# Performance work log

Hardware: AMD Instinct MI355X
Metric: run time of the kernel (lower is better)

## Reference

```python
import jax, jax.numpy as jnp
import numpy as np
from jax import lax

DT = 0.1
B, T, SD, CD, H = 1024, 200, 64, 32, 512


def setup_inputs() -> dict:
    key = jax.random.key(0)
    k0, k1, k2, k3 = jax.random.split(key, 4)
    scale1 = 1.0 / np.sqrt(SD + CD)
    scale2 = 1.0 / np.sqrt(H)
    return {
        "x0": jax.random.normal(k0, (B, SD), dtype=jnp.float32),
        "controls": jax.random.normal(k1, (B, T, CD), dtype=jnp.float32),
        "W1": jax.random.normal(k2, (SD + CD, H), dtype=jnp.float32) * scale1,
        "b1": jnp.zeros((H,), dtype=jnp.float32),
        "W2": jax.random.normal(k3, (H, SD), dtype=jnp.float32) * scale2,
        "b2": jnp.zeros((SD,), dtype=jnp.float32),
    }


def reference(x0, controls, W1, b1, W2, b2):
    # dynamics: x_{t+1} = x + dt * MLP(concat(x, u)); rollout with true data dependency
    def step(x, u):
        h = jnp.tanh(jnp.concatenate([x, u], axis=-1) @ W1 + b1)  # [B, H]
        x_next = x + DT * (h @ W2 + b2)                           # [B, SD]
        return x_next, x_next

    controls_t = jnp.swapaxes(controls, 0, 1)  # [T, B, CD]
    _, xs = lax.scan(step, x0, controls_t)     # xs: [T, B, SD]
    states = jnp.concatenate([x0[:, None, :], jnp.swapaxes(xs, 0, 1)], axis=1)  # [B, T+1, SD]
    return states
```

## Files before the change

kernel.cpp:

```cpp
#include <hip/hip_runtime.h>
#include <cstddef>


constexpr int B_  = 1024;
constexpr int T_  = 200;
constexpr int SD_ = 64;
constexpr int CD_ = 32;
constexpr int H_  = 512;
constexpr int KD_ = SD_ + CD_;
constexpr float DT_ = 0.1f;
constexpr int ROWS_ = 4;
constexpr int THREADS_ = 1024;
constexpr int KSLICES_ = 8;
constexpr int KLEN_ = KD_ / KSLICES_;

typedef float f2 __attribute__((ext_vector_type(2)));

__global__ __launch_bounds__(THREADS_)
void rollout_r15_kernel(
    const float* __restrict__ x0,
    const float* __restrict__ ctrl,
    const float* __restrict__ W1,
    const float* __restrict__ b1,
    const float* __restrict__ W2,
    const float* __restrict__ b2,
    float* __restrict__ out)
{
    __shared__ __align__(16) float xcT[KD_][ROWS_];
    __shared__ __align__(16) float part1[KSLICES_][ROWS_][H_];
    __shared__ __align__(16) float pbuf[ROWS_][H_];
    __shared__ __align__(16) float part2[ROWS_][32][SD_];

    const int tid = threadIdx.x;
    const int r0  = blockIdx.x * ROWS_;

    const int jpg   = tid & 127;
    const int ks    = tid >> 7;
    const int j0    = jpg * 2;
    const int kbase = ks * KLEN_;
    f2 w1a[KLEN_], w1b[KLEN_];
    #pragma unroll
    for (int i = 0; i < KLEN_; ++i) {
        w1a[i] = *(const f2*)&W1[(size_t)(kbase + i) * H_ + j0];
        w1b[i] = *(const f2*)&W1[(size_t)(kbase + i) * H_ + j0 + 256];
    }

    const int wv    = tid >> 6;
    const int lane  = tid & 63;
    const int l5    = lane >> 5;
    const int sfp   = lane & 31;
    const int sf0   = sfp * 2;
    const int hbase = wv * 32 + l5 * 16;
    f2 w2p[16];
    #pragma unroll
    for (int i = 0; i < 16; ++i)
        w2p[i] = *(const f2*)&W2[(size_t)(hbase + i) * SD_ + sf0];

    const int rF  = tid >> 8;
    const int jjF = (tid & 255) * 2;
    const f2 bj2 = {b1[jjF], b1[jjF + 1]};

    const int rf = (tid >> 6) & 3;
    const int sf = tid & 63;
    const float bs = b2[sf];

    const int  lt = tid - 512;
    const bool loader = (lt >= 0) && (lt < ROWS_ * CD_);
    const int  lr = (lt >> 5) & 3;
    const int  lc = lt & 31;
    const size_t ctrl_base = (size_t)(r0 + lr) * T_ * CD_ + lc;

    if (tid < ROWS_ * SD_) {
        const float v = x0[(size_t)(r0 + rf) * SD_ + sf];
        xcT[sf][rf] = v;
        out[(size_t)(r0 + rf) * (T_ + 1) * SD_ + sf] = v;
    }
    if (loader) xcT[SD_ + lc][lr] = ctrl[ctrl_base];
    __syncthreads();

    for (int t = 0; t < T_; ++t) {
        float cpre = 0.f;
        if (loader && (t + 1 < T_))
            cpre = ctrl[ctrl_base + (size_t)(t + 1) * CD_];

        f2 a0 = {0.f,0.f}, a1 = {0.f,0.f}, a2 = {0.f,0.f}, a3 = {0.f,0.f};
        f2 b0 = {0.f,0.f}, b1v = {0.f,0.f}, b2v = {0.f,0.f}, b3 = {0.f,0.f};
        #pragma unroll
        for (int i = 0; i < KLEN_; ++i) {
            const float4 xv = *(const float4*)&xcT[kbase + i][0];
            const f2 wa = w1a[i];
            const f2 wb = w1b[i];
            a0  = __builtin_elementwise_fma(wa, (f2){xv.x, xv.x}, a0);
            a1  = __builtin_elementwise_fma(wa, (f2){xv.y, xv.y}, a1);
            a2  = __builtin_elementwise_fma(wa, (f2){xv.z, xv.z}, a2);
            a3  = __builtin_elementwise_fma(wa, (f2){xv.w, xv.w}, a3);
            b0  = __builtin_elementwise_fma(wb, (f2){xv.x, xv.x}, b0);
            b1v = __builtin_elementwise_fma(wb, (f2){xv.y, xv.y}, b1v);
            b2v = __builtin_elementwise_fma(wb, (f2){xv.z, xv.z}, b2v);
            b3  = __builtin_elementwise_fma(wb, (f2){xv.w, xv.w}, b3);
        }
        *(f2*)&part1[ks][0][j0] = a0;
        *(f2*)&part1[ks][1][j0] = a1;
        *(f2*)&part1[ks][2][j0] = a2;
        *(f2*)&part1[ks][3][j0] = a3;
        *(f2*)&part1[ks][0][j0 + 256] = b0;
        *(f2*)&part1[ks][1][j0 + 256] = b1v;
        *(f2*)&part1[ks][2][j0 + 256] = b2v;
        *(f2*)&part1[ks][3][j0 + 256] = b3;
        __syncthreads();

        {
            const f2 s0 = *(const f2*)&part1[0][rF][jjF] + *(const f2*)&part1[1][rF][jjF];
            const f2 s1 = *(const f2*)&part1[2][rF][jjF] + *(const f2*)&part1[3][rF][jjF];
            const f2 s2 = *(const f2*)&part1[4][rF][jjF] + *(const f2*)&part1[5][rF][jjF];
            const f2 s3 = *(const f2*)&part1[6][rF][jjF] + *(const f2*)&part1[7][rF][jjF];
            const f2 s  = ((s0 + s1) + (s2 + s3)) + bj2;
            f2 hv;
            hv.x = tanhf(s.x);
            hv.y = tanhf(s.y);
            *(f2*)&pbuf[rF][jjF] = hv;
            if (loader && (t + 1 < T_))
                xcT[SD_ + lc][lr] = cpre;
        }
        __syncthreads();

        {
            f2 q0 = {0.f,0.f}, q1 = {0.f,0.f}, q2 = {0.f,0.f}, q3 = {0.f,0.f};
            #pragma unroll
            for (int i4 = 0; i4 < 16; i4 += 4) {
                const float4 h0 = *(const float4*)&pbuf[0][hbase + i4];
                const float4 h1 = *(const float4*)&pbuf[1][hbase + i4];
                const float4 h2 = *(const float4*)&pbuf[2][hbase + i4];
                const float4 h3 = *(const float4*)&pbuf[3][hbase + i4];
                q0 = __builtin_elementwise_fma((f2){h0.x, h0.x}, w2p[i4 + 0], q0);
                q0 = __builtin_elementwise_fma((f2){h0.y, h0.y}, w2p[i4 + 1], q0);
                q0 = __builtin_elementwise_fma((f2){h0.z, h0.z}, w2p[i4 + 2], q0);
                q0 = __builtin_elementwise_fma((f2){h0.w, h0.w}, w2p[i4 + 3], q0);
                q1 = __builtin_elementwise_fma((f2){h1.x, h1.x}, w2p[i4 + 0], q1);
                q1 = __builtin_elementwise_fma((f2){h1.y, h1.y}, w2p[i4 + 1], q1);
                q1 = __builtin_elementwise_fma((f2){h1.z, h1.z}, w2p[i4 + 2], q1);
                q1 = __builtin_elementwise_fma((f2){h1.w, h1.w}, w2p[i4 + 3], q1);
                q2 = __builtin_elementwise_fma((f2){h2.x, h2.x}, w2p[i4 + 0], q2);
                q2 = __builtin_elementwise_fma((f2){h2.y, h2.y}, w2p[i4 + 1], q2);
                q2 = __builtin_elementwise_fma((f2){h2.z, h2.z}, w2p[i4 + 2], q2);
                q2 = __builtin_elementwise_fma((f2){h2.w, h2.w}, w2p[i4 + 3], q2);
                q3 = __builtin_elementwise_fma((f2){h3.x, h3.x}, w2p[i4 + 0], q3);
                q3 = __builtin_elementwise_fma((f2){h3.y, h3.y}, w2p[i4 + 1], q3);
                q3 = __builtin_elementwise_fma((f2){h3.z, h3.z}, w2p[i4 + 2], q3);
                q3 = __builtin_elementwise_fma((f2){h3.w, h3.w}, w2p[i4 + 3], q3);
            }
            const int c = wv * 2 + l5;
            *(f2*)&part2[0][c][sf0] = q0;
            *(f2*)&part2[1][c][sf0] = q1;
            *(f2*)&part2[2][c][sf0] = q2;
            *(f2*)&part2[3][c][sf0] = q3;
        }
        __syncthreads();

        if (tid < ROWS_ * SD_) {
            float v[32];
            #pragma unroll
            for (int c = 0; c < 32; ++c) v[c] = part2[rf][c][sf];
            float s[8];
            #pragma unroll
            for (int c = 0; c < 8; ++c)
                s[c] = (v[4*c] + v[4*c+1]) + (v[4*c+2] + v[4*c+3]);
            const float acc = ((s[0] + s[1]) + (s[2] + s[3]))
                            + ((s[4] + s[5]) + (s[6] + s[7]));
            const float xnew = xcT[sf][rf] + DT_ * (acc + bs);
            xcT[sf][rf] = xnew;
            out[(size_t)(r0 + rf) * (T_ + 1) * SD_ + (size_t)(t + 1) * SD_ + sf] = xnew;
        }
        __syncthreads();
    }
}

extern "C" void kernel_launch(void* const* d_in, const int* in_sizes, int n_in,
                              void* d_out, int out_size, void* d_ws, size_t ws_size,
                              hipStream_t stream) {
    const float* x0   = (const float*)d_in[0];
    const float* ctrl = (const float*)d_in[1];
    const float* W1   = (const float*)d_in[2];
    const float* b1   = (const float*)d_in[3];
    const float* W2   = (const float*)d_in[4];
    const float* b2   = (const float*)d_in[5];
    float* out = (float*)d_out;

    dim3 grid(B_ / ROWS_);
    dim3 block(THREADS_);
    rollout_r15_kernel<<<grid, block, 0, stream>>>(x0, ctrl, W1, b1, W2, b2, out);
}
```

Before: 664.2 us.

## Halve rows per block to two and launch 512-thread blocks

Each block now handles 2 batch rows with 512 threads instead of 4 rows with 1024 threads, so the grid doubles to 512 blocks. To keep coverage, each thread holds four W1 column pairs and 32 W2 rows in registers. The aim is to put two independent blocks on each CU so one block's barrier stalls and serial per-step latency can overlap with the other's work. The cost is more per-thread register pressure and twice as many blocks streaming the weights from global memory into registers.

```diff
diff --git a/kernel.cpp b/kernel.cpp
--- a/kernel.cpp
+++ b/kernel.cpp
@@ -9,15 +9,16 @@
 constexpr int H_  = 512;
 constexpr int KD_ = SD_ + CD_;
 constexpr float DT_ = 0.1f;
-constexpr int ROWS_ = 4;
-constexpr int THREADS_ = 1024;
+constexpr int ROWS_ = 2;
+constexpr int THREADS_ = 512;
 constexpr int KSLICES_ = 8;
 constexpr int KLEN_ = KD_ / KSLICES_;
+constexpr int JREP_ = 4;
 
 typedef float f2 __attribute__((ext_vector_type(2)));
 
 __global__ __launch_bounds__(THREADS_)
-void rollout_r15_kernel(
+void rollout_r16_kernel(
     const float* __restrict__ x0,
     const float* __restrict__ ctrl,
     const float* __restrict__ W1,
@@ -29,44 +30,44 @@
     __shared__ __align__(16) float xcT[KD_][ROWS_];
     __shared__ __align__(16) float part1[KSLICES_][ROWS_][H_];
     __shared__ __align__(16) float pbuf[ROWS_][H_];
-    __shared__ __align__(16) float part2[ROWS_][32][SD_];
+    __shared__ __align__(16) float part2[ROWS_][16][SD_];
 
     const int tid = threadIdx.x;
     const int r0  = blockIdx.x * ROWS_;
 
-    const int jpg   = tid & 127;
-    const int ks    = tid >> 7;
+    const int jpg   = tid & 63;
+    const int ks    = tid >> 6;
     const int j0    = jpg * 2;
     const int kbase = ks * KLEN_;
-    f2 w1a[KLEN_], w1b[KLEN_];
+    f2 w1p[JREP_][KLEN_];
     #pragma unroll
-    for (int i = 0; i < KLEN_; ++i) {
-        w1a[i] = *(const f2*)&W1[(size_t)(kbase + i) * H_ + j0];
-        w1b[i] = *(const f2*)&W1[(size_t)(kbase + i) * H_ + j0 + 256];
-    }
+    for (int m = 0; m < JREP_; ++m)
+        #pragma unroll
+        for (int i = 0; i < KLEN_; ++i)
+            w1p[m][i] = *(const f2*)&W1[(size_t)(kbase + i) * H_ + j0 + 128 * m];
 
     const int wv    = tid >> 6;
     const int lane  = tid & 63;
     const int l5    = lane >> 5;
     const int sfp   = lane & 31;
     const int sf0   = sfp * 2;
-    const int hbase = wv * 32 + l5 * 16;
-    f2 w2p[16];
+    const int hbase = wv * 64 + l5 * 32;
+    f2 w2p[32];
     #pragma unroll
-    for (int i = 0; i < 16; ++i)
+    for (int i = 0; i < 32; ++i)
         w2p[i] = *(const f2*)&W2[(size_t)(hbase + i) * SD_ + sf0];
 
     const int rF  = tid >> 8;
     const int jjF = (tid & 255) * 2;
     const f2 bj2 = {b1[jjF], b1[jjF + 1]};
 
-    const int rf = (tid >> 6) & 3;
+    const int rf = (tid >> 6) & 1;
     const int sf = tid & 63;
     const float bs = b2[sf];
 
-    const int  lt = tid - 512;
+    const int  lt = tid - 256;
     const bool loader = (lt >= 0) && (lt < ROWS_ * CD_);
-    const int  lr = (lt >> 5) & 3;
+    const int  lr = (lt >> 5) & 1;
     const int  lc = lt & 31;
     const size_t ctrl_base = (size_t)(r0 + lr) * T_ * CD_ + lc;
 
@@ -83,30 +84,27 @@
         if (loader && (t + 1 < T_))
             cpre = ctrl[ctrl_base + (size_t)(t + 1) * CD_];
 
-        f2 a0 = {0.f,0.f}, a1 = {0.f,0.f}, a2 = {0.f,0.f}, a3 = {0.f,0.f};
-        f2 b0 = {0.f,0.f}, b1v = {0.f,0.f}, b2v = {0.f,0.f}, b3 = {0.f,0.f};
+        f2 acc[ROWS_][JREP_];
+        #pragma unroll
+        for (int r = 0; r < ROWS_; ++r)
+            #pragma unroll
+            for (int m = 0; m < JREP_; ++m)
+                acc[r][m] = (f2){0.f, 0.f};
         #pragma unroll
         for (int i = 0; i < KLEN_; ++i) {
-            const float4 xv = *(const float4*)&xcT[kbase + i][0];
-            const f2 wa = w1a[i];
-            const f2 wb = w1b[i];
-            a0  = __builtin_elementwise_fma(wa, (f2){xv.x, xv.x}, a0);
-            a1  = __builtin_elementwise_fma(wa, (f2){xv.y, xv.y}, a1);
-            a2  = __builtin_elementwise_fma(wa, (f2){xv.z, xv.z}, a2);
-            a3  = __builtin_elementwise_fma(wa, (f2){xv.w, xv.w}, a3);
-            b0  = __builtin_elementwise_fma(wb, (f2){xv.x, xv.x}, b0);
-            b1v = __builtin_elementwise_fma(wb, (f2){xv.y, xv.y}, b1v);
-            b2v = __builtin_elementwise_fma(wb, (f2){xv.z, xv.z}, b2v);
-            b3  = __builtin_elementwise_fma(wb, (f2){xv.w, xv.w}, b3);
+            const f2 xv = *(const f2*)&xcT[kbase + i][0];
+            #pragma unroll
+            for (int m = 0; m < JREP_; ++m) {
+                const f2 w = w1p[m][i];
+                acc[0][m] = __builtin_elementwise_fma(w, (f2){xv.x, xv.x}, acc[0][m]);
+                acc[1][m] = __builtin_elementwise_fma(w, (f2){xv.y, xv.y}, acc[1][m]);
+            }
         }
-        *(f2*)&part1[ks][0][j0] = a0;
-        *(f2*)&part1[ks][1][j0] = a1;
-        *(f2*)&part1[ks][2][j0] = a2;
-        *(f2*)&part1[ks][3][j0] = a3;
-        *(f2*)&part1[ks][0][j0 + 256] = b0;
-        *(f2*)&part1[ks][1][j0 + 256] = b1v;
-        *(f2*)&part1[ks][2][j0 + 256] = b2v;
-        *(f2*)&part1[ks][3][j0 + 256] = b3;
+        #pragma unroll
+        for (int m = 0; m < JREP_; ++m) {
+            *(f2*)&part1[ks][0][j0 + 128 * m] = acc[0][m];
+            *(f2*)&part1[ks][1][j0 + 128 * m] = acc[1][m];
+        }
         __syncthreads();
 
         {
@@ -125,13 +123,11 @@
         __syncthreads();
 
         {
-            f2 q0 = {0.f,0.f}, q1 = {0.f,0.f}, q2 = {0.f,0.f}, q3 = {0.f,0.f};
+            f2 q0 = {0.f, 0.f}, q1 = {0.f, 0.f};
             #pragma unroll
-            for (int i4 = 0; i4 < 16; i4 += 4) {
+            for (int i4 = 0; i4 < 32; i4 += 4) {
                 const float4 h0 = *(const float4*)&pbuf[0][hbase + i4];
                 const float4 h1 = *(const float4*)&pbuf[1][hbase + i4];
-                const float4 h2 = *(const float4*)&pbuf[2][hbase + i4];
-                const float4 h3 = *(const float4*)&pbuf[3][hbase + i4];
                 q0 = __builtin_elementwise_fma((f2){h0.x, h0.x}, w2p[i4 + 0], q0);
                 q0 = __builtin_elementwise_fma((f2){h0.y, h0.y}, w2p[i4 + 1], q0);
                 q0 = __builtin_elementwise_fma((f2){h0.z, h0.z}, w2p[i4 + 2], q0);
@@ -140,34 +136,23 @@
                 q1 = __builtin_elementwise_fma((f2){h1.y, h1.y}, w2p[i4 + 1], q1);
                 q1 = __builtin_elementwise_fma((f2){h1.z, h1.z}, w2p[i4 + 2], q1);
                 q1 = __builtin_elementwise_fma((f2){h1.w, h1.w}, w2p[i4 + 3], q1);
-                q2 = __builtin_elementwise_fma((f2){h2.x, h2.x}, w2p[i4 + 0], q2);
-                q2 = __builtin_elementwise_fma((f2){h2.y, h2.y}, w2p[i4 + 1], q2);
-                q2 = __builtin_elementwise_fma((f2){h2.z, h2.z}, w2p[i4 + 2], q2);
-                q2 = __builtin_elementwise_fma((f2){h2.w, h2.w}, w2p[i4 + 3], q2);
-                q3 = __builtin_elementwise_fma((f2){h3.x, h3.x}, w2p[i4 + 0], q3);
-                q3 = __builtin_elementwise_fma((f2){h3.y, h3.y}, w2p[i4 + 1], q3);
-                q3 = __builtin_elementwise_fma((f2){h3.z, h3.z}, w2p[i4 + 2], q3);
-                q3 = __builtin_elementwise_fma((f2){h3.w, h3.w}, w2p[i4 + 3], q3);
             }
             const int c = wv * 2 + l5;
             *(f2*)&part2[0][c][sf0] = q0;
             *(f2*)&part2[1][c][sf0] = q1;
-            *(f2*)&part2[2][c][sf0] = q2;
-            *(f2*)&part2[3][c][sf0] = q3;
         }
         __syncthreads();
 
         if (tid < ROWS_ * SD_) {
-            float v[32];
+            float v[16];
             #pragma unroll
-            for (int c = 0; c < 32; ++c) v[c] = part2[rf][c][sf];
-            float s[8];
-            #pragma unroll
-            for (int c = 0; c < 8; ++c)
-                s[c] = (v[4*c] + v[4*c+1]) + (v[4*c+2] + v[4*c+3]);
-            const float acc = ((s[0] + s[1]) + (s[2] + s[3]))
-                            + ((s[4] + s[5]) + (s[6] + s[7]));
-            const float xnew = xcT[sf][rf] + DT_ * (acc + bs);
+            for (int c = 0; c < 16; ++c) v[c] = part2[rf][c][sf];
+            const float s0 = (v[0] + v[1]) + (v[2] + v[3]);
+            const float s1 = (v[4] + v[5]) + (v[6] + v[7]);
+            const float s2 = (v[8] + v[9]) + (v[10] + v[11]);
+            const float s3 = (v[12] + v[13]) + (v[14] + v[15]);
+            const float acc2 = (s0 + s1) + (s2 + s3);
+            const float xnew = xcT[sf][rf] + DT_ * (acc2 + bs);
             xcT[sf][rf] = xnew;
             out[(size_t)(r0 + rf) * (T_ + 1) * SD_ + (size_t)(t + 1) * SD_ + sf] = xnew;
         }
@@ -188,5 +173,5 @@
 
     dim3 grid(B_ / ROWS_);
     dim3 block(THREADS_);
-    rollout_r15_kernel<<<grid, block, 0, stream>>>(x0, ctrl, W1, b1, W2, b2, out);
+    rollout_r16_kernel<<<grid, block, 0, stream>>>(x0, ctrl, W1, b1, W2, b2, out);
 }
```

Result: slower. 754.2 us (+13.6%).
